# Performance work log

Measured on AMD Instinct MI355X. Metric: run time of the kernel, lower is better.

The kernel has to match this reference:

```python
import jax, jax.numpy as jnp
import numpy as np
from jax import lax

B, IN_N, OUT_N, SEQ, HID = 8, 16, 16, 256, 64
NUM_C = 64 + 3  # grid_size + spline_order
EPS_LN = 1e-5


def setup_inputs():
    key = jax.random.key(0)
    k = jax.random.split(key, 8)
    f32 = jnp.float32
    return {
        "x_in": jax.random.normal(k[0], (B, IN_N, SEQ, HID), f32),
        "proj_x_prev": jax.random.normal(k[1], (B, IN_N, SEQ, HID), f32),
        "spline_weights": jax.random.normal(k[2], (IN_N, OUT_N, NUM_C), f32) * 0.1,
        "base_scales": 0.6 + 0.1 * jax.random.normal(k[3], (IN_N, OUT_N), f32),
        "tau": jax.random.normal(k[4], (IN_N, OUT_N), f32) * 0.1 + 0.1,
        "temperature": jnp.array(1.0, f32),
        "omiga": jnp.full((IN_N, OUT_N), 0.2, f32),
        "W2": jax.random.normal(k[5], (OUT_N, HID, HID), f32) / np.sqrt(HID).astype(np.float32),
        "b_param": jnp.zeros((OUT_N, SEQ, HID), f32),
        "ln_w": jnp.ones((OUT_N, HID), f32),
        "ln_b": jnp.zeros((OUT_N, HID), f32),
        "alpha": jnp.full((OUT_N,), 0.5, f32),
        "beta": jnp.ones((OUT_N,), f32),
        "gamma": jnp.full((OUT_N,), 0.5, f32),
        "theta": jnp.ones((OUT_N,), f32),
        "conv_w": jax.random.normal(k[6], (OUT_N, HID, 1, 3, 3), f32) * 0.1,
    }


def _layernorm(x, w=None, b=None):
    mu = jnp.mean(x, -1, keepdims=True)
    var = jnp.mean((x - mu) ** 2, -1, keepdims=True)
    y = (x - mu) / jnp.sqrt(var + EPS_LN)
    if w is not None:
        y = y * w + b
    return y


def _dwconv(x, w):
    # x: [b, C, 16, 16]; w: [C, 1, 3, 3]; depthwise conv, SAME padding
    return lax.conv_general_dilated(
        x, w, (1, 1), "SAME",
        dimension_numbers=("NCHW", "OIHW", "NCHW"),
        feature_group_count=x.shape[1])


def _forward(x_in, proj_x_prev, spline_weights, base_scales, tau, temperature,
             omiga, W2, b_param, ln_w, ln_b, alpha, beta, gamma, theta, conv_w):
    b, in_n, seq, feat = x_in.shape
    num_c = spline_weights.shape[-1]
    grid = jnp.linspace(-1.0, 1.0, num_c)
    h = 2.0 / (num_c - 1)

    x_energy = jnp.mean(x_in, -1)  # [b,i,s]
    x_norm = jnp.clip(
        x_energy / (jnp.max(jnp.abs(x_energy), -1, keepdims=True) + 1e-8),
        -0.99, 0.99)

    # cubic B-spline basis (masked branches -> nested where)
    dist = jnp.abs(x_norm[..., None] - grid) / h  # [b,i,s,c]
    basis = jnp.where(dist < 1.0, 2.0 / 3.0 - dist ** 2 + dist ** 3 / 2.0,
            jnp.where(dist < 2.0, (2.0 - dist) ** 3 / 6.0, jnp.zeros_like(dist)))

    base_feat = jax.nn.silu(x_norm)[:, :, None, :] * base_scales[None, :, :, None]  # [b,i,j,s]
    spline_feat = jnp.einsum("bisc,ijc->bijs", basis, spline_weights)
    edge_resp = base_feat + spline_feat
    # [b,i,j,s,f]
    activated = (edge_resp[..., None] + jnp.abs(omiga)[None, :, :, None, None]) * x_in[:, :, None]

    t_val = jnp.abs(temperature) + 1e-4
    edge_energies = jnp.mean(jnp.abs(activated), axis=(-1, -2))  # [b,i,j]
    tau_abs = jnp.abs(tau)  # [i,j]
    mask = jax.nn.sigmoid((edge_energies - tau_abs[None]) / t_val)  # [b,i,j]

    # attention kernel W1, vectorized over output neuron j
    mid = in_n // 2
    mult = edge_energies / (tau_abs[None] + 1e-8)  # [b,i,j]
    wp = proj_x_prev[:, :, None] * (mult * mask)[..., None, None]  # [b,i,j,s,d]
    d = wp.shape[-1]
    K = jnp.transpose(wp[:, :mid], (0, 2, 3, 1, 4)).reshape(b, -1, seq, mid * d)
    Q = jnp.transpose(wp[:, mid:2 * mid], (0, 2, 3, 1, 4)).reshape(b, -1, seq, mid * d)
    K, Q = _layernorm(K), _layernorm(Q)
    raw = jnp.einsum("bjsk,bjtk->bjst", K, Q) / (jnp.sqrt(jnp.float32(mid * d)) * t_val)
    W1 = jax.nn.softmax(raw, axis=-1)  # [b,j,s,s]

    # masked mean over input neurons -> per-neuron SplineWeightLayer (vectorized)
    x = jnp.mean(activated * mask[..., None, None], axis=1)  # [b,j,s,f]
    xn = _layernorm(x, ln_w[None, :, None, :], ln_b[None, :, None, :])
    x_prime = jnp.einsum("bjsf,jfo->bjso", xn, W2) + b_param[None]  # [b,j,s,o]
    o = x_prime.shape[-1]

    # depthwise 3x3 conv on 16x16 spatial view, per-j kernels
    xsp = jnp.transpose(x_prime, (1, 0, 3, 2)).reshape(-1, b, o, 16, 16)  # [j,b,o,16,16]
    w3 = jax.vmap(_dwconv)(xsp, conv_w)  # [j,b,o,16,16]
    w3 = jnp.transpose(w3.reshape(-1, b, o, seq), (1, 0, 3, 2))  # [b,j,s,o]

    eye = jnp.eye(seq, dtype=x_prime.dtype)
    ak = (jnp.abs(beta)[None, :, None, None] * W1
          + jnp.abs(alpha)[None, :, None, None] * eye[None, None])
    glob = jnp.einsum("bjst,bjto->bjso", ak, x_prime)
    combined = glob + jnp.abs(theta)[None, :, None, None] * w3
    # residual_proj is Identity since in_hidden == out_hidden
    out = combined + gamma[None, :, None, None] * x
    return out, x_prime  # both [b, out_n, seq, out_hidden]


def reference(x_in, proj_x_prev, spline_weights, base_scales, tau, temperature,
              omiga, W2, b_param, ln_w, ln_b, alpha, beta, gamma, theta, conv_w):
    return _forward(x_in, proj_x_prev, spline_weights, base_scales, tau, temperature,
                    omiga, W2, b_param, ln_w, ln_b, alpha, beta, gamma, theta, conv_w)
```

## Files before the change

### kernel.cpp

```cpp
#include <hip/hip_runtime.h>

#define EPSLN 1e-5f

typedef short bf16x8 __attribute__((ext_vector_type(8)));
typedef float f32x4 __attribute__((ext_vector_type(4)));
typedef unsigned short u16;
typedef unsigned short u16x8 __attribute__((ext_vector_type(8)));

__device__ __forceinline__ float wsum(float v){
  #pragma unroll
  for(int o=32;o;o>>=1) v += __shfl_xor(v,o);
  return v;
}
__device__ __forceinline__ float wmax(float v){
  #pragma unroll
  for(int o=32;o;o>>=1) v = fmaxf(v,__shfl_xor(v,o));
  return v;
}
__device__ __forceinline__ u16 f2bf(float f){
  unsigned int u = __float_as_uint(f);
  u = (u + 0x7FFFu + ((u>>16)&1u)) >> 16;
  return (u16)u;
}
__device__ __forceinline__ float bf2f(u16 h){
  return __uint_as_float(((unsigned int)h)<<16);
}

__global__ void __launch_bounds__(256) kA(
                   const float* __restrict__ xin, const float* __restrict__ p,
                   const float* __restrict__ W2,
                   float* __restrict__ xe, float* __restrict__ xa,
                   float* __restrict__ Sv, float* __restrict__ SSv,
                   u16* __restrict__ xinb, u16* __restrict__ phi, u16* __restrict__ plo,
                   u16* __restrict__ w2B){
  int t = threadIdx.x;
  int rl = t>>3, q = t&7;
  int row = blockIdx.x*32 + rl;
  const float4* xr = (const float4*)(xin + row*64 + q*8);
  const float4* pr = (const float4*)(p   + row*64 + q*8);
  float s1=0.f,s2=0.f,s3=0.f,s4=0.f;
  u16x8 xb, ph, pl;
  #pragma unroll
  for(int k=0;k<2;k++){
    float4 xv = xr[k];
    float4 pv = pr[k];
    s1 += xv.x+xv.y+xv.z+xv.w;
    s2 += fabsf(xv.x)+fabsf(xv.y)+fabsf(xv.z)+fabsf(xv.w);
    s3 += pv.x+pv.y+pv.z+pv.w;
    s4 += pv.x*pv.x+pv.y*pv.y+pv.z*pv.z+pv.w*pv.w;
    int o = k*4;
    xb[o+0]=f2bf(xv.x); xb[o+1]=f2bf(xv.y); xb[o+2]=f2bf(xv.z); xb[o+3]=f2bf(xv.w);
    u16 h0=f2bf(pv.x), h1=f2bf(pv.y), h2=f2bf(pv.z), h3=f2bf(pv.w);
    ph[o+0]=h0; ph[o+1]=h1; ph[o+2]=h2; ph[o+3]=h3;
    pl[o+0]=f2bf(pv.x-bf2f(h0)); pl[o+1]=f2bf(pv.y-bf2f(h1));
    pl[o+2]=f2bf(pv.z-bf2f(h2)); pl[o+3]=f2bf(pv.w-bf2f(h3));
  }
  *(u16x8*)(xinb + row*64 + q*8) = xb;
  *(u16x8*)(phi  + row*64 + q*8) = ph;
  *(u16x8*)(plo  + row*64 + q*8) = pl;
  s1 += __shfl_xor(s1,1); s1 += __shfl_xor(s1,2); s1 += __shfl_xor(s1,4);
  s2 += __shfl_xor(s2,1); s2 += __shfl_xor(s2,2); s2 += __shfl_xor(s2,4);
  s3 += __shfl_xor(s3,1); s3 += __shfl_xor(s3,2); s3 += __shfl_xor(s3,4);
  s4 += __shfl_xor(s4,1); s4 += __shfl_xor(s4,2); s4 += __shfl_xor(s4,4);
  if(q==0){ xe[row]=s1*(1.f/64.f); xa[row]=s2*(1.f/64.f); Sv[row]=s3; SSv[row]=s4; }
  if(blockIdx.x<16){
    int j = blockIdx.x;
    for(int idx=threadIdx.x; idx<4096; idx+=256){
      int f = idx>>6, o = idx&63;
      float v = W2[j*4096 + idx];
      int ks = f>>5, kb = (f>>3)&3, i = f&7;
      int nt = o>>4, col = o&15;
      int ln = kb*16 + col;
      w2B[((j*2+ks)*4 + nt)*512 + ln*8 + i] = f2bf(v);
    }
  }
}

__global__ void __launch_bounds__(256) kBE(
                   const float* __restrict__ xe, const float* __restrict__ sw,
                   const float* __restrict__ bs, const float* __restrict__ om,
                   const float* __restrict__ xa, const float* __restrict__ tau,
                   const float* __restrict__ temp,
                   float* __restrict__ er2, float* __restrict__ mask,
                   float* __restrict__ cc,
                   const u16* __restrict__ phi, const u16* __restrict__ plo,
                   float* __restrict__ G){
  __shared__ __align__(16) unsigned char shm[32768];
  int tid = threadIdx.x;
  if(blockIdx.x < 128){
    float* swL = (float*)shm;
    float* bsL = swL + 1072;
    float* omL = bsL + 16;
    float* red = omL + 16;
    float* redE= red + 4;
    int bi = blockIdx.x;
    int i = bi & 15;
    int w = tid>>6, lane = tid&63;
    for(int k=tid;k<16*67;k+=256) swL[k] = sw[i*16*67 + k];
    if(tid<16){ bsL[tid]=bs[i*16+tid]; omL[tid]=fabsf(om[i*16+tid]); }
    float v = xe[bi*256+tid];
    float m = wmax(fabsf(v));
    if(lane==0) red[w]=m;
    __syncthreads();
    m = fmaxf(fmaxf(red[0],red[1]),fmaxf(red[2],red[3]));
    float xn = v/(m+1e-8f);
    xn = fminf(fmaxf(xn,-0.99f),0.99f);
    float sil = xn/(1.f+expf(-xn));
    float vv = (xn+1.f)*33.f;
    int c0 = (int)floorf(vv)-1;
    float acc[16];
    #pragma unroll
    for(int j=0;j<16;j++) acc[j]=0.f;
    #pragma unroll
    for(int k=0;k<4;k++){
      int c = c0+k;
      if(c<0||c>66) continue;
      float d = fabsf(vv-(float)c);
      float bas = d<1.f ? (2.f/3.f - d*d + d*d*d*0.5f)
                : (d<2.f ? (2.f-d)*(2.f-d)*(2.f-d)*(1.f/6.f) : 0.f);
      #pragma unroll
      for(int j=0;j<16;j++) acc[j] += bas*swL[j*67+c];
    }
    float xav = xa[bi*256+tid];
    #pragma unroll
    for(int j=0;j<16;j++){
      float ev = sil*bsL[j] + acc[j] + omL[j];
      er2[(bi*16+j)*256+tid] = ev;
      float pe = wsum(fabsf(ev)*xav);
      if(lane==0) redE[j*4+w]=pe;
    }
    __syncthreads();
    if(tid<16){
      float e = (redE[tid*4+0]+redE[tid*4+1]+redE[tid*4+2]+redE[tid*4+3])*(1.f/256.f);
      float tv = fabsf(temp[0])+1e-4f;
      float ta = fabsf(tau[i*16+tid]);
      float mk = 1.f/(1.f+expf(-(e-ta)/tv));
      mask[bi*16+tid]=mk;
      cc[bi*16+tid]= e/(ta+1e-8f)*mk;
    }
  } else {
    u16* AfB = (u16*)shm;
    u16* BfB = AfB + 8192;
    int e = blockIdx.x - 128;
    int b = e&7, m = (e>>3)&7, sx = (e>>6)&3, ty = e>>8;
    int bm = b*8+m;
    int s0 = sx*64, t0 = ty*64;
    int row = tid>>2, dseg = tid&3;
    size_t offA = ((size_t)(b*16+m  )*256 + s0 + row)*64 + dseg*16;
    size_t offB = ((size_t)(b*16+m+8)*256 + t0 + row)*64 + dseg*16;
    int d0 = dseg*16;
    int ks0 = d0>>5, kb0 = (d0>>3)&3;
    int ks1 = (d0+8)>>5, kb1 = ((d0+8)>>3)&3;
    int lr = row&15, stile = row>>4;
    #define AOFF(h,stl,ks,ln) (((((h)*4+(stl))*2+(ks))*64 + (ln))*8)
    {
      uint4 v0 = *(const uint4*)(phi + offA);
      uint4 v1 = *(const uint4*)(phi + offA + 8);
      *(uint4*)(AfB + AOFF(0,stile,ks0,kb0*16+lr)) = v0;
      *(uint4*)(AfB + AOFF(0,stile,ks1,kb1*16+lr)) = v1;
      uint4 w0 = *(const uint4*)(plo + offA);
      uint4 w1 = *(const uint4*)(plo + offA + 8);
      *(uint4*)(AfB + AOFF(1,stile,ks0,kb0*16+lr)) = w0;
      *(uint4*)(AfB + AOFF(1,stile,ks1,kb1*16+lr)) = w1;
      uint4 x0 = *(const uint4*)(phi + offB);
      uint4 x1 = *(const uint4*)(phi + offB + 8);
      *(uint4*)(BfB + AOFF(0,stile,ks0,kb0*16+lr)) = x0;
      *(uint4*)(BfB + AOFF(0,stile,ks1,kb1*16+lr)) = x1;
      uint4 y0 = *(const uint4*)(plo + offB);
      uint4 y1 = *(const uint4*)(plo + offB + 8);
      *(uint4*)(BfB + AOFF(1,stile,ks0,kb0*16+lr)) = y0;
      *(uint4*)(BfB + AOFF(1,stile,ks1,kb1*16+lr)) = y1;
    }
    __syncthreads();
    int w = tid>>6, lane = tid&63;
    bf16x8 ah0 = *(const bf16x8*)(AfB + AOFF(0,w,0,lane));
    bf16x8 ah1 = *(const bf16x8*)(AfB + AOFF(0,w,1,lane));
    bf16x8 al0 = *(const bf16x8*)(AfB + AOFF(1,w,0,lane));
    bf16x8 al1 = *(const bf16x8*)(AfB + AOFF(1,w,1,lane));
    f32x4 acc[4];
    #pragma unroll
    for(int tt=0;tt<4;tt++) acc[tt] = (f32x4){0.f,0.f,0.f,0.f};
    #pragma unroll
    for(int tt=0;tt<4;tt++){
      bf16x8 bh0 = *(const bf16x8*)(BfB + AOFF(0,tt,0,lane));
      bf16x8 bh1 = *(const bf16x8*)(BfB + AOFF(0,tt,1,lane));
      bf16x8 bl0 = *(const bf16x8*)(BfB + AOFF(1,tt,0,lane));
      bf16x8 bl1 = *(const bf16x8*)(BfB + AOFF(1,tt,1,lane));
      acc[tt] = __builtin_amdgcn_mfma_f32_16x16x32_bf16(ah0, bh0, acc[tt], 0,0,0);
      acc[tt] = __builtin_amdgcn_mfma_f32_16x16x32_bf16(ah1, bh1, acc[tt], 0,0,0);
      acc[tt] = __builtin_amdgcn_mfma_f32_16x16x32_bf16(ah0, bl0, acc[tt], 0,0,0);
      acc[tt] = __builtin_amdgcn_mfma_f32_16x16x32_bf16(ah1, bl1, acc[tt], 0,0,0);
      acc[tt] = __builtin_amdgcn_mfma_f32_16x16x32_bf16(al0, bh0, acc[tt], 0,0,0);
      acc[tt] = __builtin_amdgcn_mfma_f32_16x16x32_bf16(al1, bh1, acc[tt], 0,0,0);
    }
    int col = lane&15, r4 = lane>>4;
    #pragma unroll
    for(int tt=0;tt<4;tt++){
      #pragma unroll
      for(int r=0;r<4;r++){
        G[((size_t)bm*256 + s0 + w*16 + r4*4 + r)*256 + t0 + tt*16 + col] = acc[tt][r];
      }
    }
    #undef AOFF
  }
}

__global__ void __launch_bounds__(256) kD(
                   const u16* __restrict__ xinb, const float* __restrict__ er2,
                   const float* __restrict__ mask, const u16* __restrict__ w2B,
                   const float* __restrict__ lnw, const float* __restrict__ lnb,
                   const float* __restrict__ bp,
                   u16* __restrict__ xoutb, float* __restrict__ xp,
                   u16* __restrict__ xpB){
  int b = blockIdx.x, j = blockIdx.y, st = blockIdx.z;
  int tid = threadIdx.x, w = tid>>6, lane = tid&63;
  __shared__ __align__(16) u16 xnS[16*64];
  __shared__ float mcL[16];
  if(tid<16) mcL[tid]=mask[(b*16+tid)*16+j];
  __syncthreads();
  int bj = b*16+j;
  unsigned char* xnB = (unsigned char*)xnS;
  int ss = lane>>4, fq = lane&15;
  int sl = w*4 + ss;
  int s  = st*16 + sl;
  float4 lw4 = *(const float4*)(lnw + j*64 + fq*4);
  float4 lb4 = *(const float4*)(lnb + j*64 + fq*4);
  float acc0=0.f,acc1=0.f,acc2=0.f,acc3=0.f;
  #pragma unroll
  for(int i=0;i<16;i++){
    float er = er2[((b*16+i)*16+j)*256+s]*mcL[i];
    ushort4 xv = *(const ushort4*)(xinb + ((size_t)(b*16+i)*256+s)*64 + fq*4);
    acc0 += er*bf2f(xv.x);
    acc1 += er*bf2f(xv.y);
    acc2 += er*bf2f(xv.z);
    acc3 += er*bf2f(xv.w);
  }
  acc0*=(1.f/16.f); acc1*=(1.f/16.f); acc2*=(1.f/16.f); acc3*=(1.f/16.f);
  {
    u16 pk[4]={f2bf(acc0),f2bf(acc1),f2bf(acc2),f2bf(acc3)};
    *(ushort4*)(xoutb + ((size_t)bj*256+s)*64 + fq*4) = *(ushort4*)pk;
  }
  float part = acc0+acc1+acc2+acc3;
  part += __shfl_xor(part,1); part += __shfl_xor(part,2);
  part += __shfl_xor(part,4); part += __shfl_xor(part,8);
  float mu = part*(1.f/64.f);
  float d0=acc0-mu, d1=acc1-mu, d2=acc2-mu, d3=acc3-mu;
  float p2 = d0*d0+d1*d1+d2*d2+d3*d3;
  p2 += __shfl_xor(p2,1); p2 += __shfl_xor(p2,2);
  p2 += __shfl_xor(p2,4); p2 += __shfl_xor(p2,8);
  float rstd = rsqrtf(p2*(1.f/64.f)+EPSLN);
  {
    u16 xn[4] = { f2bf(d0*rstd*lw4.x + lb4.x), f2bf(d1*rstd*lw4.y + lb4.y),
                  f2bf(d2*rstd*lw4.z + lb4.z), f2bf(d3*rstd*lw4.w + lb4.w) };
    *(ushort4*)(xnB + ((sl*128 + fq*8) ^ ((sl&7)<<4))) = *(ushort4*)xn;
  }
  __syncthreads();
  f32x4 acc = {0.f,0.f,0.f,0.f};
  int m = lane&15, kb = lane>>4;
  #pragma unroll
  for(int ks=0;ks<2;ks++){
    bf16x8 a = *(const bf16x8*)(xnB + ((m*128 + ks*64 + kb*16) ^ ((m&7)<<4)));
    bf16x8 bfr = *(const bf16x8*)(w2B + ((j*2+ks)*4 + w)*512 + lane*8);
    acc = __builtin_amdgcn_mfma_f32_16x16x32_bf16(a, bfr, acc, 0, 0, 0);
  }
  int f = w*16 + m;
  u16 pk[4];
  #pragma unroll
  for(int r=0;r<4;r++){
    int si = kb*4 + r;
    int s2 = st*16 + si;
    float xpr = acc[r] + bp[((size_t)j*256+s2)*64+f];
    xp[((size_t)bj*256+s2)*64+f] = xpr;
    pk[r] = f2bf(xpr);
  }
  int s0 = st*16 + kb*4;
  int flat = ((s0>>5)*4 + w)*512 + ((s0>>3)&3)*128 + m*8 + (s0&7);
  *(ushort4*)(xpB + (size_t)bj*16384 + flat) = *(ushort4*)pk;
}

__global__ void __launch_bounds__(256) kF(
    const float* __restrict__ G, const float* __restrict__ cc,
    const float* __restrict__ Sv, const float* __restrict__ SSv,
    const float* __restrict__ xp, const u16* __restrict__ xpB,
    const float* __restrict__ cw,
    const u16* __restrict__ xarrb, const float* __restrict__ temp,
    const float* __restrict__ alpha, const float* __restrict__ beta,
    const float* __restrict__ gamma_, const float* __restrict__ theta,
    float* __restrict__ out){
  int b = blockIdx.x, jp = blockIdx.y, st = blockIdx.z;
  int j0 = jp*4;
  int tid = threadIdx.x, w = tid>>6, lane = tid&63;
  __shared__ __align__(16) unsigned char ovl[41472];
  float* mQL = (float*)(ovl + 32768);
  float* rQL = (float*)(ovl + 36864);
  float* mKL = (float*)(ovl + 40960);
  float* rKL = (float*)(ovl + 41216);
  float* xpT = (float*)ovl;
  float tv = fabsf(temp[0])+1e-4f;
  float inv = 1.f/(sqrtf(512.f)*tv);
  float aM0[8],aM1[8],aM2[8],aM3[8];
  {
    int t = tid;
    float sk0=0,sk1=0,sk2=0,sk3=0, ssk0=0,ssk1=0,ssk2=0,ssk3=0;
    float sq0=0,sq1=0,sq2=0,sq3=0, ssq0=0,ssq1=0,ssq2=0,ssq3=0;
    #pragma unroll
    for(int m=0;m<8;m++){
      float4 ck = *(const float4*)(cc + (b*16+m  )*16 + j0);
      float4 cq = *(const float4*)(cc + (b*16+m+8)*16 + j0);
      aM0[m]=ck.x*cq.x; aM1[m]=ck.y*cq.y; aM2[m]=ck.z*cq.z; aM3[m]=ck.w*cq.w;
      float svk = Sv [(b*16+m)*256+t];
      float ssvk= SSv[(b*16+m)*256+t];
      float svq = Sv [(b*16+m+8)*256+t];
      float ssvq= SSv[(b*16+m+8)*256+t];
      sk0 += ck.x*svk; ssk0 += ck.x*ck.x*ssvk;
      sk1 += ck.y*svk; ssk1 += ck.y*ck.y*ssvk;
      sk2 += ck.z*svk; ssk2 += ck.z*ck.z*ssvk;
      sk3 += ck.w*svk; ssk3 += ck.w*ck.w*ssvk;
      sq0 += cq.x*svq; ssq0 += cq.x*cq.x*ssvq;
      sq1 += cq.y*svq; ssq1 += cq.y*cq.y*ssvq;
      sq2 += cq.z*svq; ssq2 += cq.z*cq.z*ssvq;
      sq3 += cq.w*svq; ssq3 += cq.w*cq.w*ssvq;
    }
    float mq;
    mq = sq0*(1.f/512.f); mQL[0*256+t]=mq; rQL[0*256+t]=rsqrtf(ssq0*(1.f/512.f)-mq*mq+EPSLN);
    mq = sq1*(1.f/512.f); mQL[1*256+t]=mq; rQL[1*256+t]=rsqrtf(ssq1*(1.f/512.f)-mq*mq+EPSLN);
    mq = sq2*(1.f/512.f); mQL[2*256+t]=mq; rQL[2*256+t]=rsqrtf(ssq2*(1.f/512.f)-mq*mq+EPSLN);
    mq = sq3*(1.f/512.f); mQL[3*256+t]=mq; rQL[3*256+t]=rsqrtf(ssq3*(1.f/512.f)-mq*mq+EPSLN);
    if((t>>4)==st){
      int si = t&15;
      float mk;
      mk = sk0*(1.f/512.f); mKL[0*16+si]=mk; rKL[0*16+si]=rsqrtf(ssk0*(1.f/512.f)-mk*mk+EPSLN);
      mk = sk1*(1.f/512.f); mKL[1*16+si]=mk; rKL[1*16+si]=rsqrtf(ssk1*(1.f/512.f)-mk*mk+EPSLN);
      mk = sk2*(1.f/512.f); mKL[2*16+si]=mk; rKL[2*16+si]=rsqrtf(ssk2*(1.f/512.f)-mk*mk+EPSLN);
      mk = sk3*(1.f/512.f); mKL[3*16+si]=mk; rKL[3*16+si]=rsqrtf(ssk3*(1.f/512.f)-mk*mk+EPSLN);
    }
  }
  __syncthreads();
  const float* Gb = G + (size_t)(b*8)*65536;
  float4 mQ4a = *(const float4*)&mQL[0*256+lane*4];
  float4 rQ4a = *(const float4*)&rQL[0*256+lane*4];
  float4 mQ4b = *(const float4*)&mQL[1*256+lane*4];
  float4 rQ4b = *(const float4*)&rQL[1*256+lane*4];
  float4 mQ4c = *(const float4*)&mQL[2*256+lane*4];
  float4 rQ4c = *(const float4*)&rQL[2*256+lane*4];
  float4 mQ4d = *(const float4*)&mQL[3*256+lane*4];
  float4 rQ4d = *(const float4*)&rQL[3*256+lane*4];
  #pragma unroll
  for(int q=0;q<4;q++){
    int si = w*4+q;
    int s = st*16 + si;
    f32x4 dt0={0.f,0.f,0.f,0.f}, dt1={0.f,0.f,0.f,0.f};
    f32x4 dt2={0.f,0.f,0.f,0.f}, dt3={0.f,0.f,0.f,0.f};
    #pragma unroll
    for(int m=0;m<8;m++){
      f32x4 g4 = *(const f32x4*)(Gb + (size_t)m*65536 + s*256 + lane*4);
      dt0 += aM0[m]*g4; dt1 += aM1[m]*g4;
      dt2 += aM2[m]*g4; dt3 += aM3[m]*g4;
    }
    #define SMAX(JJ, DT, MQ, RQ) { \
      float mKs = 512.f*mKL[JJ*16+si], rKs = rKL[JJ*16+si]; \
      float e0 = __expf((DT[0] - mKs*MQ.x)*rKs*RQ.x*inv); \
      float e1 = __expf((DT[1] - mKs*MQ.y)*rKs*RQ.y*inv); \
      float e2 = __expf((DT[2] - mKs*MQ.z)*rKs*RQ.z*inv); \
      float e3 = __expf((DT[3] - mKs*MQ.w)*rKs*RQ.w*inv); \
      float isf = 1.f/wsum(e0+e1+e2+e3); \
      u16 pk[4] = {f2bf(e0*isf), f2bf(e1*isf), f2bf(e2*isf), f2bf(e3*isf)}; \
      *(ushort4*)(ovl + JJ*8192 + ((si*512 + lane*8) ^ ((si&7)<<4))) = *(ushort4*)pk; }
    SMAX(0, dt0, mQ4a, rQ4a)
    SMAX(1, dt1, mQ4b, rQ4b)
    SMAX(2, dt2, mQ4c, rQ4c)
    SMAX(3, dt3, mQ4d, rQ4d)
    #undef SMAX
  }
  __syncthreads();
  int m_ = lane&15, kb = lane>>4;
  f32x4 av0={0.f,0.f,0.f,0.f}, av1={0.f,0.f,0.f,0.f};
  f32x4 av2={0.f,0.f,0.f,0.f}, av3={0.f,0.f,0.f,0.f};
  const u16* xpB0 = xpB + (size_t)(b*16+j0  )*16384;
  const u16* xpB1 = xpB + (size_t)(b*16+j0+1)*16384;
  const u16* xpB2 = xpB + (size_t)(b*16+j0+2)*16384;
  const u16* xpB3 = xpB + (size_t)(b*16+j0+3)*16384;
  #pragma unroll
  for(int ks=0;ks<8;ks++){
    int aoff = (m_*512 + ks*64 + kb*16) ^ ((m_&7)<<4);
    int boff = ((ks*4 + w)*64 + lane)*8;
    bf16x8 a0 = *(const bf16x8*)(ovl +         aoff);
    bf16x8 a1 = *(const bf16x8*)(ovl +  8192 + aoff);
    bf16x8 a2 = *(const bf16x8*)(ovl + 16384 + aoff);
    bf16x8 a3 = *(const bf16x8*)(ovl + 24576 + aoff);
    av0 = __builtin_amdgcn_mfma_f32_16x16x32_bf16(a0, *(const bf16x8*)(xpB0 + boff), av0, 0,0,0);
    av1 = __builtin_amdgcn_mfma_f32_16x16x32_bf16(a1, *(const bf16x8*)(xpB1 + boff), av1, 0,0,0);
    av2 = __builtin_amdgcn_mfma_f32_16x16x32_bf16(a2, *(const bf16x8*)(xpB2 + boff), av2, 0,0,0);
    av3 = __builtin_amdgcn_mfma_f32_16x16x32_bf16(a3, *(const bf16x8*)(xpB3 + boff), av3, 0,0,0);
  }
  int f = w*16 + m_;
  #pragma unroll
  for(int pass=0; pass<2; pass++){
    __syncthreads();
    for(int idx4 = tid; idx4 < 1536; idx4 += 256){
      int jj = idx4 / 768;
      int rem = idx4 - jj*768;
      int rr_i = rem >> 8;
      int pos = rem & 255;
      int ci = pos>>4, f4 = pos&15;
      int grow = st - 1 + rr_i;
      float4 v = {0.f,0.f,0.f,0.f};
      if(grow>=0 && grow<16){
        v = *(const float4*)(xp + ((size_t)(b*16+j0+pass*2+jj)*256 + grow*16 + ci)*64 + f4*4);
      }
      *(float4*)(xpT + ((jj*3+rr_i)*16+ci)*68 + f4*4) = v;
    }
    __syncthreads();
    #pragma unroll
    for(int jj=0;jj<2;jj++){
      int j = j0 + pass*2 + jj;
      int bj = b*16+j;
      f32x4 acc = pass==0 ? (jj?av1:av0) : (jj?av3:av2);
      float al = fabsf(alpha[j]), be=fabsf(beta[j]), th=fabsf(theta[j]), ga=gamma_[j];
      const float* wq = cw + (j*64+f)*9;
      float w0=wq[0],w1=wq[1],w2=wq[2],w3v=wq[3],w4=wq[4],w5=wq[5],w6=wq[6],w7=wq[7],w8=wq[8];
      #pragma unroll
      for(int r=0;r<4;r++){
        int si = kb*4 + r;
        int s = st*16 + si;
        float gl = acc[r];
        float cv=0.f;
        #pragma unroll
        for(int dr=0;dr<3;dr++){
          float kw0 = dr==0?w0:(dr==1?w3v:w6);
          float kw1 = dr==0?w1:(dr==1?w4:w7);
          float kw2 = dr==0?w2:(dr==1?w5:w8);
          const float* rowp = xpT + ((jj*3+dr)*16)*68;
          if(si>0)  cv += rowp[(si-1)*68+f]*kw0;
                    cv += rowp[(si  )*68+f]*kw1;
          if(si<15) cv += rowp[(si+1)*68+f]*kw2;
        }
        float diag = xpT[((jj*3+1)*16+si)*68+f];
        size_t gi = ((size_t)bj*256+s)*64+f;
        out[gi] = be*gl + al*diag + th*cv + ga*bf2f(xarrb[gi]);
      }
    }
  }
}

extern "C" void kernel_launch(void* const* d_in, const int* in_sizes, int n_in,
                              void* d_out, int out_size, void* d_ws, size_t ws_size,
                              hipStream_t stream) {
  const float* xin = (const float*)d_in[0];
  const float* pxp = (const float*)d_in[1];
  const float* sw  = (const float*)d_in[2];
  const float* bs  = (const float*)d_in[3];
  const float* tau = (const float*)d_in[4];
  const float* temp= (const float*)d_in[5];
  const float* om  = (const float*)d_in[6];
  const float* W2  = (const float*)d_in[7];
  const float* bp  = (const float*)d_in[8];
  const float* lnw = (const float*)d_in[9];
  const float* lnb = (const float*)d_in[10];
  const float* alpha=(const float*)d_in[11];
  const float* beta= (const float*)d_in[12];
  const float* gam = (const float*)d_in[13];
  const float* theta=(const float*)d_in[14];
  const float* cw  = (const float*)d_in[15];
  float* outp = (float*)d_out;
  float* xpo  = outp + 2097152;

  float* ws  = (float*)d_ws;
  float* xe  = ws;
  float* xa  = xe + 32768;
  float* Sv  = xa + 32768;
  float* SSv = Sv + 32768;
  float* er2 = SSv + 32768;
  float* mask= er2 + 524288;
  float* ccv = mask + 2048;
  float* Gv  = ccv + 2048;
  u16* xvb = (u16*)(Gv + 4194304);
  u16* xpB = xvb + 2097152;
  u16* w2B = xpB + 2097152;
  u16* xinb= w2B + 65536;
  u16* phi = xinb + 2097152;
  u16* plo = phi + 2097152;

  kA<<<1024,256,0,stream>>>(xin,pxp,W2,xe,xa,Sv,SSv,xinb,phi,plo,w2B);
  kBE<<<1152,256,0,stream>>>(xe,sw,bs,om,xa,tau,temp,er2,mask,ccv,phi,plo,Gv);
  kD<<<dim3(8,16,16),256,0,stream>>>(xinb,er2,mask,w2B,lnw,lnb,bp,xvb,xpo,xpB);
  kF<<<dim3(8,4,16),256,0,stream>>>(Gv,ccv,Sv,SSv,xpo,xpB,cw,xvb,temp,
                                    alpha,beta,gam,theta,outp);
}
```

Baseline: 56.47 us.

## Store er2 as bf16 and halve kF softmax LDS by two-phase staging

The intermediate er2 tensor moves from fp32 to bf16, which halves its write traffic in kBE and its read traffic in kD. In kF, the four per-j softmax probability tiles no longer all sit in LDS at once. Two are stored and consumed by MFMA, then the other two (held in registers) are written into the same buffers. This cuts shared memory from about 41KB to 26KB to allow more resident blocks, at the cost of extra barriers, more register pressure and bf16 rounding of er2.

```diff
diff --git a/kernel.cpp b/kernel.cpp
--- a/kernel.cpp
+++ b/kernel.cpp
@@ -81,7 +81,7 @@
                    const float* __restrict__ bs, const float* __restrict__ om,
                    const float* __restrict__ xa, const float* __restrict__ tau,
                    const float* __restrict__ temp,
-                   float* __restrict__ er2, float* __restrict__ mask,
+                   u16* __restrict__ er2b, float* __restrict__ mask,
                    float* __restrict__ cc,
                    const u16* __restrict__ phi, const u16* __restrict__ plo,
                    float* __restrict__ G){
@@ -125,7 +125,7 @@
     #pragma unroll
     for(int j=0;j<16;j++){
       float ev = sil*bsL[j] + acc[j] + omL[j];
-      er2[(bi*16+j)*256+tid] = ev;
+      er2b[(bi*16+j)*256+tid] = f2bf(ev);
       float pe = wsum(fabsf(ev)*xav);
       if(lane==0) redE[j*4+w]=pe;
     }
@@ -206,7 +206,7 @@
 }
 
 __global__ void __launch_bounds__(256) kD(
-                   const u16* __restrict__ xinb, const float* __restrict__ er2,
+                   const u16* __restrict__ xinb, const u16* __restrict__ er2b,
                    const float* __restrict__ mask, const u16* __restrict__ w2B,
                    const float* __restrict__ lnw, const float* __restrict__ lnb,
                    const float* __restrict__ bp,
@@ -228,7 +228,7 @@
   float acc0=0.f,acc1=0.f,acc2=0.f,acc3=0.f;
   #pragma unroll
   for(int i=0;i<16;i++){
-    float er = er2[((b*16+i)*16+j)*256+s]*mcL[i];
+    float er = bf2f(er2b[((b*16+i)*16+j)*256+s])*mcL[i];
     ushort4 xv = *(const ushort4*)(xinb + ((size_t)(b*16+i)*256+s)*64 + fq*4);
     acc0 += er*bf2f(xv.x);
     acc1 += er*bf2f(xv.y);
@@ -290,11 +290,13 @@
   int b = blockIdx.x, jp = blockIdx.y, st = blockIdx.z;
   int j0 = jp*4;
   int tid = threadIdx.x, w = tid>>6, lane = tid&63;
-  __shared__ __align__(16) unsigned char ovl[41472];
-  float* mQL = (float*)(ovl + 32768);
-  float* rQL = (float*)(ovl + 36864);
-  float* mKL = (float*)(ovl + 40960);
-  float* rKL = (float*)(ovl + 41216);
+  __shared__ __align__(16) unsigned char ovl[26112];
+  unsigned char* prA = ovl;
+  unsigned char* prB = ovl + 8192;
+  float* mQL = (float*)(ovl + 16384);
+  float* rQL = (float*)(ovl + 20480);
+  float* mKL = (float*)(ovl + 24576);
+  float* rKL = (float*)(ovl + 24832);
   float* xpT = (float*)ovl;
   float tv = fabsf(temp[0])+1e-4f;
   float inv = 1.f/(sqrtf(512.f)*tv);
@@ -345,6 +347,7 @@
   float4 rQ4c = *(const float4*)&rQL[2*256+lane*4];
   float4 mQ4d = *(const float4*)&mQL[3*256+lane*4];
   float4 rQ4d = *(const float4*)&rQL[3*256+lane*4];
+  ushort4 pk2[4], pk3[4];
   #pragma unroll
   for(int q=0;q<4;q++){
     int si = w*4+q;
@@ -357,7 +360,7 @@
       dt0 += aM0[m]*g4; dt1 += aM1[m]*g4;
       dt2 += aM2[m]*g4; dt3 += aM3[m]*g4;
     }
-    #define SMAX(JJ, DT, MQ, RQ) { \
+    #define SMK(JJ, DT, MQ, RQ, PKOUT) { \
       float mKs = 512.f*mKL[JJ*16+si], rKs = rKL[JJ*16+si]; \
       float e0 = __expf((DT[0] - mKs*MQ.x)*rKs*RQ.x*inv); \
       float e1 = __expf((DT[1] - mKs*MQ.y)*rKs*RQ.y*inv); \
@@ -365,12 +368,16 @@
       float e3 = __expf((DT[3] - mKs*MQ.w)*rKs*RQ.w*inv); \
       float isf = 1.f/wsum(e0+e1+e2+e3); \
       u16 pk[4] = {f2bf(e0*isf), f2bf(e1*isf), f2bf(e2*isf), f2bf(e3*isf)}; \
-      *(ushort4*)(ovl + JJ*8192 + ((si*512 + lane*8) ^ ((si&7)<<4))) = *(ushort4*)pk; }
-    SMAX(0, dt0, mQ4a, rQ4a)
-    SMAX(1, dt1, mQ4b, rQ4b)
-    SMAX(2, dt2, mQ4c, rQ4c)
-    SMAX(3, dt3, mQ4d, rQ4d)
-    #undef SMAX
+      PKOUT = *(ushort4*)pk; }
+    ushort4 t0v, t1v;
+    SMK(0, dt0, mQ4a, rQ4a, t0v)
+    SMK(1, dt1, mQ4b, rQ4b, t1v)
+    int poff = (si*512 + lane*8) ^ ((si&7)<<4);
+    *(ushort4*)(prA + poff) = t0v;
+    *(ushort4*)(prB + poff) = t1v;
+    SMK(2, dt2, mQ4c, rQ4c, pk2[q])
+    SMK(3, dt3, mQ4d, rQ4d, pk3[q])
+    #undef SMK
   }
   __syncthreads();
   int m_ = lane&15, kb = lane>>4;
@@ -384,12 +391,26 @@
   for(int ks=0;ks<8;ks++){
     int aoff = (m_*512 + ks*64 + kb*16) ^ ((m_&7)<<4);
     int boff = ((ks*4 + w)*64 + lane)*8;
-    bf16x8 a0 = *(const bf16x8*)(ovl +         aoff);
-    bf16x8 a1 = *(const bf16x8*)(ovl +  8192 + aoff);
-    bf16x8 a2 = *(const bf16x8*)(ovl + 16384 + aoff);
-    bf16x8 a3 = *(const bf16x8*)(ovl + 24576 + aoff);
+    bf16x8 a0 = *(const bf16x8*)(prA + aoff);
+    bf16x8 a1 = *(const bf16x8*)(prB + aoff);
     av0 = __builtin_amdgcn_mfma_f32_16x16x32_bf16(a0, *(const bf16x8*)(xpB0 + boff), av0, 0,0,0);
     av1 = __builtin_amdgcn_mfma_f32_16x16x32_bf16(a1, *(const bf16x8*)(xpB1 + boff), av1, 0,0,0);
+  }
+  __syncthreads();
+  #pragma unroll
+  for(int q=0;q<4;q++){
+    int si = w*4+q;
+    int poff = (si*512 + lane*8) ^ ((si&7)<<4);
+    *(ushort4*)(prA + poff) = pk2[q];
+    *(ushort4*)(prB + poff) = pk3[q];
+  }
+  __syncthreads();
+  #pragma unroll
+  for(int ks=0;ks<8;ks++){
+    int aoff = (m_*512 + ks*64 + kb*16) ^ ((m_&7)<<4);
+    int boff = ((ks*4 + w)*64 + lane)*8;
+    bf16x8 a2 = *(const bf16x8*)(prA + aoff);
+    bf16x8 a3 = *(const bf16x8*)(prB + aoff);
     av2 = __builtin_amdgcn_mfma_f32_16x16x32_bf16(a2, *(const bf16x8*)(xpB2 + boff), av2, 0,0,0);
     av3 = __builtin_amdgcn_mfma_f32_16x16x32_bf16(a3, *(const bf16x8*)(xpB3 + boff), av3, 0,0,0);
   }
@@ -470,8 +491,8 @@
   float* xa  = xe + 32768;
   float* Sv  = xa + 32768;
   float* SSv = Sv + 32768;
-  float* er2 = SSv + 32768;
-  float* mask= er2 + 524288;
+  u16*   er2b= (u16*)(SSv + 32768);
+  float* mask= (float*)(er2b) + 524288;
   float* ccv = mask + 2048;
   float* Gv  = ccv + 2048;
   u16* xvb = (u16*)(Gv + 4194304);
@@ -482,8 +503,8 @@
   u16* plo = phi + 2097152;
 
   kA<<<1024,256,0,stream>>>(xin,pxp,W2,xe,xa,Sv,SSv,xinb,phi,plo,w2B);
-  kBE<<<1152,256,0,stream>>>(xe,sw,bs,om,xa,tau,temp,er2,mask,ccv,phi,plo,Gv);
-  kD<<<dim3(8,16,16),256,0,stream>>>(xinb,er2,mask,w2B,lnw,lnb,bp,xvb,xpo,xpB);
+  kBE<<<1152,256,0,stream>>>(xe,sw,bs,om,xa,tau,temp,er2b,mask,ccv,phi,plo,Gv);
+  kD<<<dim3(8,16,16),256,0,stream>>>(xinb,er2b,mask,w2B,lnw,lnb,bp,xvb,xpo,xpB);
   kF<<<dim3(8,4,16),256,0,stream>>>(Gv,ccv,Sv,SSv,xpo,xpB,cw,xvb,temp,
                                     alpha,beta,gam,theta,outp);
 }
```

Measured after the change: 55.26 us. 2.1% less time.
